# Kernel optimization log

Measured on AMD Instinct MI355X. Metric: run time of the kernel, lower is better.

Reference implementation:

```python
import jax, jax.numpy as jnp
import numpy as np

MARGIN = 0.3   # init margin
NUMBER = 1024  # OHEM: number of hardest losses to mine
N, D = 8192, 128


def setup_inputs() -> dict:
    key = jax.random.key(0)
    k1, k2 = jax.random.split(key)
    pair1 = jax.random.normal(k1, (N, D), dtype=jnp.float32)
    pair2 = jax.random.normal(k2, (N, D), dtype=jnp.float32)
    return {"pair1": pair1, "pair2": pair2}


def _pairwise_losses(pair1, pair2):
    # d[i, j] = ||pair1[i] - pair2[j]||^2 via GEMM expansion
    sq1 = jnp.sum(pair1 * pair1, axis=1)            # [N]
    sq2 = jnp.sum(pair2 * pair2, axis=1)            # [N]
    cross = pair1 @ pair2.T                          # [N, N]
    d = sq1[:, None] + sq2[None, :] - 2.0 * cross    # [N, N]
    dist_ap = jnp.diagonal(d)                        # [N], ||pair1[i]-pair2[i]||^2
    loss = jax.nn.relu(dist_ap[:, None] - d + MARGIN)  # [N, N]
    offdiag = ~jnp.eye(d.shape[0], dtype=bool)       # i == j is skipped
    return loss, offdiag


def reference(pair1, pair2):
    loss, offdiag = _pairwise_losses(pair1, pair2)
    n = loss.shape[0]
    cnt = 2 * n * (n - 1)  # original appends each (i, j) loss twice
    # all_loss: mean over all 2*N*(N-1) (duplicated) losses
    all_loss = 2.0 * jnp.sum(jnp.where(offdiag, loss, 0.0)) / cnt
    # OHEM: top NUMBER losses over the duplicated candidate set
    flat = jnp.where(offdiag, loss, -1.0).ravel()    # sentinel -1 masks diagonal
    flat2 = jnp.concatenate([flat, flat])            # each loss appears twice
    topv, _ = jax.lax.top_k(flat2, NUMBER)
    pos = topv > 0.0
    avg_num = jnp.sum(pos)
    avg_sum = jnp.sum(jnp.where(pos, topv, 0.0))
    # if no positive loss among the mined set, fall back to the single largest loss
    avg_loss = jnp.where(avg_num > 0, avg_sum / jnp.maximum(avg_num, 1).astype(topv.dtype), topv[0])
    return avg_loss, all_loss
```

## Files before the change

### kernel.cpp

```cpp
#include <hip/hip_runtime.h>
#include <stdint.h>


#define NROWS 8192
#define DDIM  128
#define MARGIN_F 0.3f
#define HALFK 512
#define SUBCAP 8192
#define SHIST_BINS 1024

typedef unsigned short u16;
typedef short bf16x8 __attribute__((ext_vector_type(8)));
typedef float f32x4 __attribute__((ext_vector_type(4)));

#define OFF_P1B  0
#define OFF_P2B  (2*1024*1024)
#define OFF_AARR (4*1024*1024)
#define OFF_BARR (OFF_AARR + 32768)
#define OFF_MISC (OFF_AARR + 65536)
#define OFF_CAND (OFF_MISC + 8192)

__global__ void init_kernel(int* zbase) {
    const int n = 1232;
    for (int i = threadIdx.x; i < n; i += blockDim.x) zbase[i] = 0;
}

__device__ __forceinline__ u16 f2bf(float f) {
    unsigned int u = __float_as_uint(f);
    u = (u + 0x7FFFu + ((u >> 16) & 1u)) >> 16;
    return (u16)u;
}
__device__ __forceinline__ float bf2f(u16 u) {
    return __uint_as_float(((unsigned int)u) << 16);
}

__global__ __launch_bounds__(256) void prep_kernel(
    const float* __restrict__ p1, const float* __restrict__ p2,
    u16* __restrict__ p1b, u16* __restrict__ p2b,
    float* __restrict__ aArr, float* __restrict__ bArr)
{
    const int wid = threadIdx.x >> 6, lane = threadIdx.x & 63;
    const int row = blockIdx.x*4 + wid;
    const float2 v1 = *(const float2*)&p1[row*DDIM + lane*2];
    const float2 v2 = *(const float2*)&p2[row*DDIM + lane*2];
    p1b[row*DDIM + lane*2]     = f2bf(v1.x);
    p1b[row*DDIM + lane*2 + 1] = f2bf(v1.y);
    p2b[row*DDIM + lane*2]     = f2bf(v2.x);
    p2b[row*DDIM + lane*2 + 1] = f2bf(v2.y);
    float sq = v2.x*v2.x + v2.y*v2.y;
    float cp = v1.x*v2.x + v1.y*v2.y;
    #pragma unroll
    for (int off = 32; off > 0; off >>= 1) {
        sq += __shfl_down(sq, off);
        cp += __shfl_down(cp, off);
    }
    if (lane == 0) {
        bArr[row] = sq;
        aArr[row] = sq - 2.0f*cp + MARGIN_F;
    }
}

__global__ __launch_bounds__(256) void sample_kernel(
    const u16* __restrict__ p1b, const u16* __restrict__ p2b,
    const float* __restrict__ aArr, const float* __restrict__ bArr,
    int* __restrict__ shist)
{
    __shared__ float p1row[DDIM];
    __shared__ int h[SHIST_BINS];
    const int b = blockIdx.x;
    const int i = (b >> 3)*1024 + 512;
    const int j0 = (b & 7)*1024;
    const int tid = threadIdx.x;
    for (int k = tid; k < SHIST_BINS; k += 256) h[k] = 0;
    if (tid < DDIM) p1row[tid] = bf2f(p1b[i*DDIM + tid]);
    __syncthreads();
    const float ai = aArr[i];
    #pragma unroll
    for (int jj = 0; jj < 4; ++jj) {
        const int j = j0 + jj*256 + tid;
        const u16* prow = &p2b[j*DDIM];
        float dot = 0.f;
        for (int k = 0; k < DDIM; k += 8) {
            uint4 q = *(const uint4*)&prow[k];
            const u16* e = (const u16*)&q;
            #pragma unroll
            for (int t = 0; t < 8; ++t) dot += p1row[k + t] * bf2f(e[t]);
        }
        float v = ai - bArr[j] + 2.0f*dot;
        if (j != i && v > 0.f) {
            int bin = (int)(v * 4.0f);
            if (bin > SHIST_BINS - 1) bin = SHIST_BINS - 1;
            atomicAdd(&h[bin], 1);
        }
    }
    __syncthreads();
    for (int k = tid; k < SHIST_BINS; k += 256) if (h[k]) atomicAdd(&shist[k], h[k]);
}

__global__ __launch_bounds__(256) void pick_kernel(
    const int* __restrict__ shist, float* __restrict__ Tv)
{
    __shared__ int h[SHIST_BINS];
    __shared__ int chunk[256];
    const int tid = threadIdx.x;
    #pragma unroll
    for (int k = 0; k < 4; ++k) h[tid + k*256] = shist[tid + k*256];
    __syncthreads();
    int cs = 0;
    #pragma unroll
    for (int k = 0; k < 4; ++k) cs += h[tid*4 + k];
    chunk[tid] = cs;
    __syncthreads();
    if (tid == 0) {
        int run = 0, tc = -1;
        for (int t = 255; t >= 0; --t) {
            if (run + chunk[t] >= 8) { tc = t; break; }
            run += chunk[t];
        }
        float t0 = 0.f;
        if (tc >= 0) {
            int b = tc*4 + 3;
            for (; b >= tc*4; --b) { run += h[b]; if (run >= 8) break; }
            if (b < tc*4) b = tc*4;
            while (run > 24 && run - h[b] >= 8 && b < SHIST_BINS - 1) { run -= h[b]; b++; }
            t0 = 0.25f * (float)b;
        }
        *Tv = t0;
    }
}

__global__ __launch_bounds__(256, 2) void pair_gemm(
    const u16* __restrict__ p1b, const u16* __restrict__ p2b,
    const float* __restrict__ aArr, const float* __restrict__ bArr,
    const float* __restrict__ Tv,
    float* __restrict__ pS, int* __restrict__ pP,
    int* __restrict__ candCnt, float* __restrict__ cand)
{
    __shared__ u16 At[128][136];
    __shared__ u16 Bt[128][136];
    __shared__ float sredS[4];
    __shared__ int   sredP[4];
    const int tid = threadIdx.x;
    const int bi = blockIdx.y, bj = blockIdx.x;
    const int i0 = bi*128, j0 = bj*128;
    const float T0 = *Tv;
    #pragma unroll
    for (int it = 0; it < 8; ++it) {
        int c = tid + it*256;
        int r = c >> 4, cc = (c & 15) * 8;
        *(uint4*)&At[r][cc] = *(const uint4*)&p1b[(i0 + r)*DDIM + cc];
        *(uint4*)&Bt[r][cc] = *(const uint4*)&p2b[(j0 + r)*DDIM + cc];
    }
    __syncthreads();
    const int lane = tid & 63, wid = tid >> 6;
    const int r16 = lane & 15, hi = lane >> 4;
    const int wm = (wid >> 1)*64, wn = (wid & 1)*64;
    f32x4 acc[4][4];
    #pragma unroll
    for (int a = 0; a < 4; ++a)
        #pragma unroll
        for (int b = 0; b < 4; ++b) acc[a][b] = (f32x4){0.f, 0.f, 0.f, 0.f};
    #pragma unroll
    for (int ks = 0; ks < 4; ++ks) {
        const int kc = ks*32 + hi*8;
        bf16x8 aF[4], bF[4];
        #pragma unroll
        for (int mi = 0; mi < 4; ++mi) aF[mi] = *(const bf16x8*)&At[wm + mi*16 + r16][kc];
        #pragma unroll
        for (int ni = 0; ni < 4; ++ni) bF[ni] = *(const bf16x8*)&Bt[wn + ni*16 + r16][kc];
        #pragma unroll
        for (int mi = 0; mi < 4; ++mi)
            #pragma unroll
            for (int ni = 0; ni < 4; ++ni)
                acc[mi][ni] = __builtin_amdgcn_mfma_f32_16x16x32_bf16(aF[mi], bF[ni], acc[mi][ni], 0, 0, 0);
    }
    float bv[4], av[4][4];
    #pragma unroll
    for (int ni = 0; ni < 4; ++ni) bv[ni] = bArr[j0 + wn + ni*16 + r16];
    #pragma unroll
    for (int mi = 0; mi < 4; ++mi)
        #pragma unroll
        for (int r = 0; r < 4; ++r) av[mi][r] = aArr[i0 + wm + mi*16 + hi*4 + r];
    const int copy = (bi ^ bj) & 63;
    int*   myCnt  = &candCnt[copy];
    float* myCand = &cand[(size_t)copy * SUBCAP];
    float lsum = 0.f; int pcnt = 0;
    #pragma unroll
    for (int mi = 0; mi < 4; ++mi) {
        #pragma unroll
        for (int ni = 0; ni < 4; ++ni) {
            const bool hasDiag = (i0 + wm + mi*16) == (j0 + wn + ni*16);
            #pragma unroll
            for (int r = 0; r < 4; ++r) {
                const float v = av[mi][r] - bv[ni] + 2.0f*acc[mi][ni][r];
                lsum += fmaxf(v, 0.f);
                pcnt += (v > 0.f) ? 1 : 0;
                bool ok = (v >= T0);
                if (hasDiag && (hi*4 + r) == r16) ok = false;
                if (ok) {
                    int idx = atomicAdd(myCnt, 1);
                    if (idx < SUBCAP) myCand[idx] = v;
                }
            }
        }
    }
    #pragma unroll
    for (int off = 32; off > 0; off >>= 1) {
        lsum += __shfl_down(lsum, off);
        pcnt += __shfl_down(pcnt, off);
    }
    if (lane == 0) { sredS[wid] = lsum; sredP[wid] = pcnt; }
    __syncthreads();
    if (tid == 0) {
        atomicAdd(&pS[copy], sredS[0] + sredS[1] + sredS[2] + sredS[3]);
        atomicAdd(&pP[copy], sredP[0] + sredP[1] + sredP[2] + sredP[3]);
    }
}

__device__ __forceinline__ float block_reduce1024(float v, float* red, int tid) {
    #pragma unroll
    for (int off = 32; off > 0; off >>= 1) v += __shfl_down(v, off);
    __syncthreads();
    if ((tid & 63) == 0) red[tid >> 6] = v;
    __syncthreads();
    if (tid == 0) {
        float t = 0.f;
        #pragma unroll
        for (int w = 0; w < 16; ++w) t += red[w];
        red[0] = t;
    }
    __syncthreads();
    return red[0];
}

__global__ __launch_bounds__(1024) void select_kernel(
    const float* __restrict__ pS, const int* __restrict__ pP,
    const int* __restrict__ candCnt, const float* __restrict__ cand,
    const float* __restrict__ Tv, float* __restrict__ out)
{
    __shared__ int h1[1024];
    __shared__ int h2[1024];
    __shared__ float red[16];
    __shared__ int ints[8];
    __shared__ float fl[2];
    __shared__ float lst[4096];
    const int tid = threadIdx.x;
    for (int k = tid; k < 1024; k += 1024) { h1[k] = 0; h2[k] = 0; }
    if (tid == 0) {
        double sd = 0.0; int p = 0, c = 0;
        for (int k = 0; k < 64; ++k) {
            sd += (double)pS[k];
            p += pP[k];
            int cc = candCnt[k];
            c += (cc > SUBCAP ? SUBCAP : cc);
        }
        sd -= (double)NROWS * (double)MARGIN_F;
        if (sd < 0.0) sd = 0.0;
        p -= NROWS;
        if (p < 0) p = 0;
        ints[0] = p; ints[1] = c; ints[6] = 0;
        fl[0] = (float)sd;
    }
    __syncthreads();
    const int P = ints[0], C = ints[1];
    const float S = fl[0];
    const float all_loss = S * (1.0f / 67100672.0f);
    const float lo = *Tv;
    float avg = 0.f;

    if (P == 0) {
        avg = 0.f;
    } else if (P < HALFK) {
        avg = S / (float)P;
    } else if (C < HALFK) {
        float s = 0.f;
        for (int c = 0; c < 64; ++c) {
            int n = min(candCnt[c], SUBCAP);
            for (int k = tid; k < n; k += 1024) s += cand[(size_t)c*SUBCAP + k];
        }
        s = block_reduce1024(s, red, tid);
        avg = (C > 0) ? (s + (float)(HALFK - C)*lo) / (float)HALFK : 0.f;
    } else {
        for (int c = 0; c < 64; ++c) {
            int n = min(candCnt[c], SUBCAP);
            for (int k = tid; k < n; k += 1024) {
                float v = cand[(size_t)c*SUBCAP + k];
                int b = (int)((v - lo) * 0.25f);
                b = b < 0 ? 0 : (b > 1023 ? 1023 : b);
                atomicAdd(&h1[b], 1);
            }
        }
        __syncthreads();
        if (tid == 0) {
            int run = 0;
            for (int b = 1023; b >= 0; --b) {
                run += h1[b];
                if (run >= HALFK) { ints[2] = b; ints[3] = HALFK - (run - h1[b]); break; }
            }
        }
        __syncthreads();
        const int b1 = ints[2], needK = ints[3];
        const float lo2 = lo + (float)b1 * 4.0f;
        float s1 = 0.f;
        for (int c = 0; c < 64; ++c) {
            int n = min(candCnt[c], SUBCAP);
            for (int k = tid; k < n; k += 1024) {
                float v = cand[(size_t)c*SUBCAP + k];
                int b = (int)((v - lo) * 0.25f);
                b = b < 0 ? 0 : (b > 1023 ? 1023 : b);
                if (b > b1) s1 += v;
                else if (b == b1) {
                    int sb = (int)((v - lo2) * 256.0f);
                    sb = sb < 0 ? 0 : (sb > 1023 ? 1023 : sb);
                    atomicAdd(&h2[sb], 1);
                }
            }
        }
        s1 = block_reduce1024(s1, red, tid);
        if (tid == 0) {
            int run = 0;
            for (int b = 1023; b >= 0; --b) {
                run += h2[b];
                if (run >= needK) { ints[4] = b; ints[5] = needK - (run - h2[b]); break; }
            }
        }
        __syncthreads();
        const int b2 = ints[4], need3 = ints[5];
        float s2 = 0.f;
        for (int c = 0; c < 64; ++c) {
            int n = min(candCnt[c], SUBCAP);
            for (int k = tid; k < n; k += 1024) {
                float v = cand[(size_t)c*SUBCAP + k];
                int b = (int)((v - lo) * 0.25f);
                b = b < 0 ? 0 : (b > 1023 ? 1023 : b);
                if (b == b1) {
                    int sb = (int)((v - lo2) * 256.0f);
                    sb = sb < 0 ? 0 : (sb > 1023 ? 1023 : sb);
                    if (sb > b2) s2 += v;
                    else if (sb == b2) {
                        int idx = atomicAdd(&ints[6], 1);
                        if (idx < 4096) lst[idx] = v;
                    }
                }
            }
        }
        s2 = block_reduce1024(s2, red, tid);
        __syncthreads();
        const int m = min(ints[6], 4096);
        float s3 = 0.f;
        for (int k = tid; k < m; k += 1024) {
            float v = lst[k]; int g = 0;
            for (int j = 0; j < m; ++j) {
                float u = lst[j];
                g += (u > v) || (u == v && j < k);
            }
            if (g < need3) s3 += v;
        }
        s3 = block_reduce1024(s3, red, tid);
        avg = (s1 + s2 + s3) * (1.0f / (float)HALFK);
    }
    if (tid == 0) { out[0] = avg; out[1] = all_loss; }
}

extern "C" void kernel_launch(void* const* d_in, const int* in_sizes, int n_in,
                              void* d_out, int out_size, void* d_ws, size_t ws_size,
                              hipStream_t stream)
{
    const float* p1 = (const float*)d_in[0];
    const float* p2 = (const float*)d_in[1];
    char* ws = (char*)d_ws;
    u16*   p1b  = (u16*)(ws + OFF_P1B);
    u16*   p2b  = (u16*)(ws + OFF_P2B);
    float* aArr = (float*)(ws + OFF_AARR);
    float* bArr = (float*)(ws + OFF_BARR);
    int*   misc = (int*)(ws + OFF_MISC);
    int*   shist = misc;
    float* pS   = (float*)(misc + 1024);
    int*   pP   = misc + 1088;
    int*   cCnt = misc + 1152;
    float* Tv   = (float*)(misc + 1216);
    float* cand = (float*)(ws + OFF_CAND);
    float* out  = (float*)d_out;

    init_kernel<<<1, 256, 0, stream>>>(misc);
    prep_kernel<<<NROWS/4, 256, 0, stream>>>(p1, p2, p1b, p2b, aArr, bArr);
    sample_kernel<<<64, 256, 0, stream>>>(p1b, p2b, aArr, bArr, shist);
    pick_kernel<<<1, 256, 0, stream>>>(shist, Tv);
    dim3 grid(64, 64);
    pair_gemm<<<grid, 256, 0, stream>>>(p1b, p2b, aArr, bArr, Tv, pS, pP, cCnt, cand);
    select_kernel<<<1, 1024, 0, stream>>>(pS, pP, cCnt, cand, Tv, out);
}
```

Baseline: 382.6 us.

## Stream A rows per wave from global with B tile in LDS; fold init into prep

The pair GEMM now stages only the 128-column B tile in shared memory. Each wave walks 128 rows of pair1 in 16-row steps, loading A fragments straight from global memory into registers, so the grid shrinks to 64x16 blocks of 512 rows each. Candidate-buffer slots are now chosen per wave. The separate zeroing kernel is merged into the first block of prep_kernel, which saves one launch. The aims are to halve LDS footprint, raise occupancy and reuse the B tile more. The cost is uncoalesced-ish global A loads that depend on L2 hits, and a non-unrolled outer loop.

```diff
diff --git a/kernel.cpp b/kernel.cpp
--- a/kernel.cpp
+++ b/kernel.cpp
@@ -20,11 +20,6 @@
 #define OFF_MISC (OFF_AARR + 65536)
 #define OFF_CAND (OFF_MISC + 8192)
 
-__global__ void init_kernel(int* zbase) {
-    const int n = 1232;
-    for (int i = threadIdx.x; i < n; i += blockDim.x) zbase[i] = 0;
-}
-
 __device__ __forceinline__ u16 f2bf(float f) {
     unsigned int u = __float_as_uint(f);
     u = (u + 0x7FFFu + ((u >> 16) & 1u)) >> 16;
@@ -37,8 +32,12 @@
 __global__ __launch_bounds__(256) void prep_kernel(
     const float* __restrict__ p1, const float* __restrict__ p2,
     u16* __restrict__ p1b, u16* __restrict__ p2b,
-    float* __restrict__ aArr, float* __restrict__ bArr)
-{
+    float* __restrict__ aArr, float* __restrict__ bArr,
+    int* __restrict__ misc)
+{
+    if (blockIdx.x == 0) {
+        for (int i = threadIdx.x; i < 1232; i += 256) misc[i] = 0;
+    }
     const int wid = threadIdx.x >> 6, lane = threadIdx.x & 63;
     const int row = blockIdx.x*4 + wid;
     const float2 v1 = *(const float2*)&p1[row*DDIM + lane*2];
@@ -129,70 +128,70 @@
     }
 }
 
-__global__ __launch_bounds__(256, 2) void pair_gemm(
+__global__ __launch_bounds__(256) void pair_gemm(
     const u16* __restrict__ p1b, const u16* __restrict__ p2b,
     const float* __restrict__ aArr, const float* __restrict__ bArr,
     const float* __restrict__ Tv,
     float* __restrict__ pS, int* __restrict__ pP,
     int* __restrict__ candCnt, float* __restrict__ cand)
 {
-    __shared__ u16 At[128][136];
     __shared__ u16 Bt[128][136];
     __shared__ float sredS[4];
     __shared__ int   sredP[4];
     const int tid = threadIdx.x;
-    const int bi = blockIdx.y, bj = blockIdx.x;
-    const int i0 = bi*128, j0 = bj*128;
+    const int bj = blockIdx.x;
+    const int gi = blockIdx.y;
+    const int j0 = bj*128;
     const float T0 = *Tv;
     #pragma unroll
     for (int it = 0; it < 8; ++it) {
         int c = tid + it*256;
         int r = c >> 4, cc = (c & 15) * 8;
-        *(uint4*)&At[r][cc] = *(const uint4*)&p1b[(i0 + r)*DDIM + cc];
         *(uint4*)&Bt[r][cc] = *(const uint4*)&p2b[(j0 + r)*DDIM + cc];
     }
     __syncthreads();
-    const int lane = tid & 63, wid = tid >> 6;
+    const int lane = tid & 63, w = tid >> 6;
     const int r16 = lane & 15, hi = lane >> 4;
-    const int wm = (wid >> 1)*64, wn = (wid & 1)*64;
-    f32x4 acc[4][4];
-    #pragma unroll
-    for (int a = 0; a < 4; ++a)
-        #pragma unroll
-        for (int b = 0; b < 4; ++b) acc[a][b] = (f32x4){0.f, 0.f, 0.f, 0.f};
-    #pragma unroll
-    for (int ks = 0; ks < 4; ++ks) {
-        const int kc = ks*32 + hi*8;
-        bf16x8 aF[4], bF[4];
-        #pragma unroll
-        for (int mi = 0; mi < 4; ++mi) aF[mi] = *(const bf16x8*)&At[wm + mi*16 + r16][kc];
-        #pragma unroll
-        for (int ni = 0; ni < 4; ++ni) bF[ni] = *(const bf16x8*)&Bt[wn + ni*16 + r16][kc];
-        #pragma unroll
-        for (int mi = 0; mi < 4; ++mi)
-            #pragma unroll
-            for (int ni = 0; ni < 4; ++ni)
-                acc[mi][ni] = __builtin_amdgcn_mfma_f32_16x16x32_bf16(aF[mi], bF[ni], acc[mi][ni], 0, 0, 0);
-    }
-    float bv[4], av[4][4];
-    #pragma unroll
-    for (int ni = 0; ni < 4; ++ni) bv[ni] = bArr[j0 + wn + ni*16 + r16];
-    #pragma unroll
-    for (int mi = 0; mi < 4; ++mi)
-        #pragma unroll
-        for (int r = 0; r < 4; ++r) av[mi][r] = aArr[i0 + wm + mi*16 + hi*4 + r];
-    const int copy = (bi ^ bj) & 63;
+    const int row0 = gi*512 + w*128;
+    float bv[8];
+    #pragma unroll
+    for (int ni = 0; ni < 8; ++ni) bv[ni] = bArr[j0 + ni*16 + r16];
+    const int copy = ((bj*16 + gi)*4 + w) & 63;
     int*   myCnt  = &candCnt[copy];
     float* myCand = &cand[(size_t)copy * SUBCAP];
     float lsum = 0.f; int pcnt = 0;
-    #pragma unroll
-    for (int mi = 0; mi < 4; ++mi) {
-        #pragma unroll
-        for (int ni = 0; ni < 4; ++ni) {
-            const bool hasDiag = (i0 + wm + mi*16) == (j0 + wn + ni*16);
+
+    for (int t = 0; t < 8; ++t) {
+        const int rr = row0 + t*16;
+        bf16x8 aF[4];
+        #pragma unroll
+        for (int ks = 0; ks < 4; ++ks)
+            aF[ks] = *(const bf16x8*)&p1b[(rr + r16)*DDIM + ks*32 + hi*8];
+        float av[4];
+        #pragma unroll
+        for (int r = 0; r < 4; ++r) av[r] = aArr[rr + hi*4 + r];
+
+        f32x4 acc[8];
+        #pragma unroll
+        for (int ni = 0; ni < 8; ++ni) acc[ni] = (f32x4){0.f, 0.f, 0.f, 0.f};
+        #pragma unroll
+        for (int ks = 0; ks < 4; ++ks) {
+            const int kc = ks*32 + hi*8;
+            bf16x8 bF[8];
+            #pragma unroll
+            for (int ni = 0; ni < 8; ++ni) bF[ni] = *(const bf16x8*)&Bt[ni*16 + r16][kc];
+            #pragma unroll
+            for (int ni = 0; ni < 8; ++ni)
+                acc[ni] = __builtin_amdgcn_mfma_f32_16x16x32_bf16(aF[ks], bF[ni], acc[ni], 0, 0, 0);
+        }
+
+        const int iL = rr + hi*4;
+        #pragma unroll
+        for (int ni = 0; ni < 8; ++ni) {
+            const bool hasDiag = rr == (j0 + ni*16);
             #pragma unroll
             for (int r = 0; r < 4; ++r) {
-                const float v = av[mi][r] - bv[ni] + 2.0f*acc[mi][ni][r];
+                const float v = av[r] - bv[ni] + 2.0f*acc[ni][r];
                 lsum += fmaxf(v, 0.f);
                 pcnt += (v > 0.f) ? 1 : 0;
                 bool ok = (v >= T0);
@@ -204,12 +203,13 @@
             }
         }
     }
+
     #pragma unroll
     for (int off = 32; off > 0; off >>= 1) {
         lsum += __shfl_down(lsum, off);
         pcnt += __shfl_down(pcnt, off);
     }
-    if (lane == 0) { sredS[wid] = lsum; sredP[wid] = pcnt; }
+    if (lane == 0) { sredS[w] = lsum; sredP[w] = pcnt; }
     __syncthreads();
     if (tid == 0) {
         atomicAdd(&pS[copy], sredS[0] + sredS[1] + sredS[2] + sredS[3]);
@@ -382,11 +382,10 @@
     float* cand = (float*)(ws + OFF_CAND);
     float* out  = (float*)d_out;
 
-    init_kernel<<<1, 256, 0, stream>>>(misc);
-    prep_kernel<<<NROWS/4, 256, 0, stream>>>(p1, p2, p1b, p2b, aArr, bArr);
+    prep_kernel<<<NROWS/4, 256, 0, stream>>>(p1, p2, p1b, p2b, aArr, bArr, misc);
     sample_kernel<<<64, 256, 0, stream>>>(p1b, p2b, aArr, bArr, shist);
     pick_kernel<<<1, 256, 0, stream>>>(shist, Tv);
-    dim3 grid(64, 64);
+    dim3 grid(64, 16);
     pair_gemm<<<grid, 256, 0, stream>>>(p1b, p2b, aArr, bArr, Tv, pS, pP, cCnt, cand);
     select_kernel<<<1, 1024, 0, stream>>>(pS, pP, cCnt, cand, Tv, out);
 }
```

New measurement: 694.6 us. +81.6%, slower.
